# Optimization experiments

Measured on AMD Instinct MI355X. Metric: run time of the kernel, lower is better.

## Reference

```python
import jax, jax.numpy as jnp
import numpy as np

BETA = 0.25  # commitment_beta


def setup_inputs() -> dict:
    key = jax.random.key(0)
    k1, k2 = jax.random.split(key)
    x = jax.random.normal(k1, (16, 256, 32, 32), dtype=jnp.float32)
    # codebook weight: (n_embed + 1, embed_dim); last row is the padding idx (zeros)
    weight = jax.random.normal(k2, (8193, 256), dtype=jnp.float32) * 0.05
    weight = weight.at[-1].set(0.0)
    return {"x": x, "weight": weight}


def reference(x, weight):
    # Eval-mode forward of VectorQuantize2 (accept_image_fmap=True, no EMA update).
    B, C, H, W = x.shape
    xf = jnp.transpose(x, (0, 2, 3, 1)).reshape(B, H * W, C)  # b (h w) c
    emb = weight[:-1]  # [N, C], drop padding row
    # squared euclidean distance; argmin identical to torch.cdist argmin
    d2 = (
        jnp.sum(xf * xf, axis=-1, keepdims=True)
        - 2.0 * jnp.einsum("bnc,kc->bnk", xf, emb)
        + jnp.sum(emb * emb, axis=-1)
    )  # [B, HW, N]
    code = jnp.argmin(d2, axis=-1)  # [B, HW]
    x_q = emb[code]  # [B, HW, C]
    loss = BETA * jnp.mean((jax.lax.stop_gradient(x_q) - xf) ** 2) + jnp.mean(
        (x_q - jax.lax.stop_gradient(xf)) ** 2
    )
    # straight-through estimator
    xq_st = xf + jax.lax.stop_gradient(x_q - xf)
    xq_out = jnp.transpose(xq_st.reshape(B, H, W, C), (0, 3, 1, 2))  # b c h w
    code_out = code.reshape(B, H, W)
    return xq_out, loss, code_out
```

## Files before the change

### kernel.cpp

```cpp
#include <hip/hip_runtime.h>
#include <hip/hip_bf16.h>


#define N_ROWS   16384
#define KCODES   8192
#define DIM      256
#define LOSS_OFF 4194304
#define CODE_OFF 4194305
#define MARGIN_ACC 0.006f

typedef _Float16 half8  __attribute__((ext_vector_type(8)));
typedef _Float16 half4v __attribute__((ext_vector_type(4)));
typedef float    float4v __attribute__((ext_vector_type(4)));
typedef unsigned long long u64;

__device__ __forceinline__ unsigned umax32(unsigned a, unsigned b) { return a > b ? a : b; }
__device__ __forceinline__ unsigned umin32(unsigned a, unsigned b) { return a < b ? a : b; }
__device__ __forceinline__ void gll16(const _Float16* g, _Float16* l) {
  __builtin_amdgcn_global_load_lds((const __attribute__((address_space(1))) void*)g,
                                   (__attribute__((address_space(3))) void*)l, 16, 0, 0);
}

__device__ __forceinline__ void stage16k(const _Float16* __restrict__ g, _Float16* l, int t, int w) {
  gll16(g + t * 8,        l + w * 512);
  gll16(g + 4096 + t * 8, l + 4096 + w * 512);
}


__global__ __launch_bounds__(256) void k_prep(const float* __restrict__ x, _Float16* __restrict__ xh,
                                              const float* __restrict__ wt, _Float16* __restrict__ eh,
                                              float* __restrict__ en2c, float* __restrict__ sxxp,
                                              double* __restrict__ dacc, unsigned* __restrict__ cnt) {
  __shared__ float lsx[128 * 65];
  __shared__ __align__(16) _Float16 ls[8192];
  __shared__ float es[32];
  int t = threadIdx.x;
  int lane = t & 63, wv = t >> 6;
  int bid = blockIdx.x;
  if (bid < 512) {
    if (bid == 0 && t == 0) { dacc[0] = 0.0; *cnt = 0u; }
    int blk = bid >> 2, cc = bid & 3;
    int row0 = blk * 128;
    int b    = row0 >> 10;
    int n0   = row0 & 1023;
    const float* xb = x + (size_t)b * 262144 + n0;
    int n_l = t & 127, cg = t >> 7;
    float sxx = 0.f;
    for (int j = 0; j < 32; ++j) {
      int c = cc * 64 + cg * 32 + j;
      float v = xb[(size_t)c * 1024 + n_l];
      sxx = fmaf(v, v, sxx);
      lsx[n_l * 65 + (c & 63)] = v;
    }
    __syncthreads();
#pragma unroll
    for (int i = 0; i < 4; ++i) {
      int unit = i * 256 + t;
      int rl = unit >> 3, p = unit & 7;
      const float* src = &lsx[rl * 65 + p * 8];
      half8 h;
#pragma unroll
      for (int k2 = 0; k2 < 8; ++k2) h[k2] = (_Float16)src[k2];
      int p7 = p ^ (rl & 7);
      *(half8*)&xh[(size_t)blk * 32768 + (size_t)cc * 8192 + (size_t)rl * 64 + p7 * 8] = h;
    }
#pragma unroll
    for (int d = 32; d; d >>= 1) sxx += __shfl_xor(sxx, d);
    __syncthreads();
    if (lane == 0) lsx[wv] = sxx;
    __syncthreads();
    if (t == 0) sxxp[bid] = lsx[0] + lsx[1] + lsx[2] + lsx[3];
  } else {
    int blk  = bid - 512;
    int k0 = blk * 32;
    const float* wb = wt + (size_t)k0 * 256;
    for (int i = 0; i < 8; ++i) {
      int lin = i * 1024 + t * 4;
      float4v v = *(const float4v*)&wb[lin];
      half4v h; float ss = 0.f;
#pragma unroll
      for (int j = 0; j < 4; ++j) { h[j] = (_Float16)v[j]; ss = fmaf(v[j], v[j], ss); }
      *(half4v*)&ls[lin] = h;
#pragma unroll
      for (int d = 32; d; d >>= 1) ss += __shfl_xor(ss, d);
      if (lane == 0) es[i * 4 + wv] = ss;
    }
    __syncthreads();
    size_t tb = (size_t)(k0 >> 7) * 32768;
    for (int i = 0; i < 4; ++i) {
      int u = i * 256 + t;
      int code_l = u >> 5;
      int cu = u & 31, chunk = cu >> 3, p = cu & 7;
      int kgl = k0 + code_l;
      int kg = p ^ (kgl & 7);
      half8 h = *(half8*)&ls[code_l * 256 + chunk * 64 + kg * 8];
      *(half8*)&eh[tb + (size_t)chunk * 8192 + (size_t)(kgl & 127) * 64 + p * 8] = h;
    }
    if (t < 32) en2c[k0 + t] = 32.0f - 0.5f * es[t];
  }
}

__global__ __launch_bounds__(512, 2) void k_gemm(const _Float16* __restrict__ xh, const _Float16* __restrict__ eh,
                                                 const float* __restrict__ en2c,
                                                 u64* __restrict__ top2) {
  __shared__ __align__(16) _Float16 As[2][16384];
  __shared__ __align__(16) _Float16 Bs[2][16384];
  int t    = threadIdx.x;
  int lane = t & 63, w = t >> 6;
  int wr = w >> 2, wc = w & 3;
  int ln15 = lane & 15, q = (lane >> 4) & 3;
  int q4 = q * 4;

  int orig = (int)blockIdx.y * 32 + (int)blockIdx.x;
  int swz  = (orig & 7) * 256 + (orig >> 3);
  int bx = swz & 31;
  int by = swz >> 5;

  const _Float16* Ag0 = eh + (size_t)(2 * bx)     * 32768;
  const _Float16* Ag1 = eh + (size_t)(2 * bx + 1) * 32768;
  const _Float16* Bg0 = xh + (size_t)(2 * by)     * 32768;
  const _Float16* Bg1 = xh + (size_t)(2 * by + 1) * 32768;

  float4v acc[8][4];
#pragma unroll
  for (int mi = 0; mi < 8; ++mi) {
    float4v cin = *(const float4v*)&en2c[bx * 256 + wr * 128 + mi * 16 + q4];
#pragma unroll
    for (int ni = 0; ni < 4; ++ni) acc[mi][ni] = cin;
  }

  stage16k(Ag0, &As[0][0],    t, w);
  stage16k(Ag1, &As[0][8192], t, w);
  stage16k(Bg0, &Bs[0][0],    t, w);
  stage16k(Bg1, &Bs[0][8192], t, w);
  asm volatile("s_waitcnt vmcnt(0)" ::: "memory");
  __builtin_amdgcn_s_barrier();

#pragma unroll
  for (int kt = 0; kt < 4; ++kt) {
    const int d = kt & 1;
    const _Float16* Ac = &As[d][0];
    const _Float16* Bc = &Bs[d][0];
    _Float16* An = &As[d ^ 1][0];
    _Float16* Bn = &Bs[d ^ 1][0];
    half8 bf[4];
#pragma unroll
    for (int p = 0; p < 4; ++p) {
      const int ks = p >> 1, mih = p & 1;
      half8 af[4];
#pragma unroll
      for (int m2 = 0; m2 < 4; ++m2) {
        int rl = (mih * 4 + m2) * 16 + ln15;
        af[m2] = *(const half8*)&Ac[wr * 8192 + rl * 64 + (((ks * 4 + q) ^ (rl & 7)) * 8)];
      }
      if (mih == 0) {
#pragma unroll
        for (int ni = 0; ni < 4; ++ni) {
          int rb = (wc & 1) * 64 + ni * 16 + ln15;
          bf[ni] = *(const half8*)&Bc[(wc >> 1) * 8192 + rb * 64 + (((ks * 4 + q) ^ (rb & 7)) * 8)];
        }
      }
      if (kt < 3) {
        if (p == 0) stage16k(Ag0 + (kt + 1) * 8192, An,        t, w);
        if (p == 1) stage16k(Ag1 + (kt + 1) * 8192, An + 8192, t, w);
        if (p == 2) stage16k(Bg0 + (kt + 1) * 8192, Bn,        t, w);
        if (p == 3) stage16k(Bg1 + (kt + 1) * 8192, Bn + 8192, t, w);
      }
      __builtin_amdgcn_s_barrier();
      asm volatile("s_waitcnt lgkmcnt(0)");
      __builtin_amdgcn_s_setprio(1);
#pragma unroll
      for (int m2 = 0; m2 < 4; ++m2)
#pragma unroll
        for (int ni = 0; ni < 4; ++ni)
          acc[mih * 4 + m2][ni] =
              __builtin_amdgcn_mfma_f32_16x16x32_f16(af[m2], bf[ni], acc[mih * 4 + m2][ni], 0, 0, 0);
      __builtin_amdgcn_s_setprio(0);
      __builtin_amdgcn_s_barrier();
    }
    if (kt < 3) {
      asm volatile("s_waitcnt vmcnt(0)" ::: "memory");
      __builtin_amdgcn_sched_barrier(0);
      __builtin_amdgcn_s_barrier();
    }
  }

#pragma unroll
  for (int ni = 0; ni < 4; ++ni) {
    unsigned hi[16], lo2[16];
#pragma unroll
    for (int mi = 0; mi < 8; ++mi)
#pragma unroll
      for (int rb = 0; rb < 4; rb += 2) {
        int j = mi * 2 + (rb >> 1);
        unsigned p0 = (__float_as_uint(acc[mi][ni][rb])     & 0xFFFFFF80u) | (unsigned)(mi * 16 + q4 + rb);
        unsigned p1 = (__float_as_uint(acc[mi][ni][rb + 1]) & 0xFFFFFF80u) | (unsigned)(mi * 16 + q4 + rb + 1);
        hi[j] = umax32(p0, p1); lo2[j] = umin32(p0, p1);
      }
#pragma unroll
    for (int st = 8; st; st >>= 1)
#pragma unroll
      for (int j = 0; j < 8; ++j) if (j < st) {
        unsigned nb = umax32(hi[j], hi[j + st]);
        unsigned ns = umax32(umin32(hi[j], hi[j + st]), umax32(lo2[j], lo2[j + st]));
        hi[j] = nb; lo2[j] = ns;
      }
    unsigned b = hi[0], s = lo2[0];
#pragma unroll
    for (int dd = 16; dd < 64; dd <<= 1) {
      unsigned ob = __shfl_xor(b, dd);
      unsigned os = __shfl_xor(s, dd);
      unsigned ns = umax32(umin32(b, ob), umax32(s, os));
      b = umax32(b, ob); s = ns;
    }
    if (q == 0) {
      int row = by * 256 + wc * 64 + ni * 16 + ln15;
      top2[(size_t)(bx * 2 + wr) * 16384 + row] = ((u64)b << 32) | s;
    }
  }
}

__global__ __launch_bounds__(1024) void k_out(const u64* __restrict__ top2,
                                              const float* __restrict__ x, const float* __restrict__ w,
                                              float* __restrict__ out, const float* __restrict__ sxxp,
                                              double* __restrict__ dacc, unsigned* __restrict__ cnt) {
  __shared__ float ect[256 * 65];
  __shared__ double dpart[16];
  __shared__ unsigned oldc;
  int t    = threadIdx.x;
  int lane = t & 63, wv = t >> 6;
  int blk  = blockIdx.x;
  int row0 = blk * 64;
  int b = row0 >> 10, n0 = row0 & 1023;

  double dsum = 0.0;
  for (int j = 0; j < 4; ++j) {
    int rl  = wv * 4 + j;
    int row = row0 + rl;
    u64 e = top2[(size_t)lane * 16384 + row];
    unsigned hi = (unsigned)(e >> 32), lo = (unsigned)e;
    unsigned mx = hi;
#pragma unroll
    for (int d = 1; d < 64; d <<= 1) mx = umax32(mx, __shfl_xor(mx, d));
    float fm = __uint_as_float(mx & 0xFFFFFF80u);
    float th = fm - MARGIN_ACC;
    bool c0 = __uint_as_float(hi & 0xFFFFFF80u) >= th;
    bool c1 = __uint_as_float(lo & 0xFFFFFF80u) >= th;
    u64 bal0 = __ballot(c0), bal1 = __ballot(c1);
    int kbest;
    double d2c;
    if (__popcll(bal0) + __popcll(bal1) <= 1) {
      int l0 = __ffsll((unsigned long long)__ballot(hi == mx)) - 1;
      kbest = l0 * 128 + (int)(__shfl(hi, l0) & 127u);
      d2c = 64.0 - 2.0 * (double)fm;
    } else {
      const float* xr = x + (size_t)b * 262144 + (row & 1023);
      float4v ex;
#pragma unroll
      for (int i = 0; i < 4; ++i) ex[i] = xr[(size_t)(lane * 4 + i) * 1024];
      double bs = 1e300; int bk = 0x7fffffff;
      for (int pass = 0; pass < 2; ++pass) {
        u64 bal = pass ? bal1 : bal0;
        unsigned src = pass ? lo : hi;
        while (bal) {
          int l = __ffsll((unsigned long long)bal) - 1;
          bal &= bal - 1;
          int kc = l * 128 + (int)(__shfl(src, l) & 127u);
          float4v wv4 = *(const float4v*)&w[(size_t)kc * DIM + lane * 4];
          double s = 0.0;
#pragma unroll
          for (int i = 0; i < 4; ++i) { double ev = (double)wv4[i]; s += ev * (ev - 2.0 * (double)ex[i]); }
#pragma unroll
          for (int d = 1; d < 64; d <<= 1) s += __shfl_xor(s, d);
          if (s < bs || (s == bs && kc < bk)) { bs = s; bk = kc; }
        }
      }
      kbest = bk;
      d2c = bs;
    }
    if (lane == 0) { out[CODE_OFF + row] = (float)kbest; dsum += d2c; }
    const float* wrow = w + (size_t)kbest * 256;
#pragma unroll
    for (int i = 0; i < 4; ++i) ect[(i * 64 + lane) * 65 + rl] = wrow[i * 64 + lane];
  }
  __syncthreads();

  const size_t base = (size_t)b * 262144 + n0 + lane;
  for (int j = 0; j < 16; ++j) {
    int c = wv * 16 + j;
    out[base + (size_t)c * 1024] = ect[c * 65 + lane];
  }
  if (lane == 0) dpart[wv] = dsum;
  __syncthreads();
  if (t == 0) {
    double s = 0.0;
#pragma unroll
    for (int i = 0; i < 16; ++i) s += dpart[i];
    atomicAdd(&dacc[0], s);
    __threadfence();
    oldc = atomicAdd(cnt, 1u);
  }
  __syncthreads();
  if (oldc == 255u && t < 64) {
    float ps = 0.f;
#pragma unroll
    for (int i = 0; i < 8; ++i) ps += sxxp[t * 8 + i];
#pragma unroll
    for (int d = 32; d; d >>= 1) ps += __shfl_xor(ps, d);
    if (t == 0) {
      __threadfence();
      double sd2 = *(volatile double*)&dacc[0];
      out[LOSS_OFF] = (float)(1.25 * ((double)ps + sd2) / 4194304.0);
    }
  }
}

extern "C" void kernel_launch(void* const* d_in, const int* in_sizes, int n_in,
                              void* d_out, int out_size, void* d_ws, size_t ws_size,
                              hipStream_t stream) {
  const float* x = (const float*)d_in[0];
  const float* w = (const float*)d_in[1];
  float* out = (float*)d_out;
  char* ws = (char*)d_ws;
  _Float16* xh   = (_Float16*)(ws);
  _Float16* eh   = (_Float16*)(ws + 8388608);
  float*    en2c = (float*)(ws + 12582912);
  u64*      top2 = (u64*)(ws + 12615680);
  float*    sxxp = (float*)(ws + 21004288);
  double*   dacc = (double*)(ws + 21006336);
  unsigned* cnt  = (unsigned*)(ws + 21006344);

  k_prep<<<768, 256, 0, stream>>>(x, xh, w, eh, en2c, sxxp, dacc, cnt);
  k_gemm<<<dim3(32, 64), 512, 0, stream>>>(xh, eh, en2c, top2);
  k_out<<<256, 1024, 0, stream>>>(top2, x, w, out, sxxp, dacc, cnt);
}
```

Baseline: 186.2 us.

## Make GEMM persistent over eight row tiles with cross-tile prefetch

The distance GEMM now launches 256 persistent blocks instead of 2048. Each block keeps one codebook column tile and loops over eight row tiles assigned by XCD index. The next tile's A and B panels are prefetched during the last k-step of the current tile, which hides per-block launch and prologue costs. Separately, the prep kernel loads x as float2 pairs to widen global loads. The persistent form reloads the A panel for every tile and may leave CUs underused if 256 blocks at 2 per CU do not balance well.

```diff
diff --git a/kernel.cpp b/kernel.cpp
--- a/kernel.cpp
+++ b/kernel.cpp
@@ -12,6 +12,7 @@
 typedef _Float16 half8  __attribute__((ext_vector_type(8)));
 typedef _Float16 half4v __attribute__((ext_vector_type(4)));
 typedef float    float4v __attribute__((ext_vector_type(4)));
+typedef float    float2v __attribute__((ext_vector_type(2)));
 typedef unsigned long long u64;
 
 __device__ __forceinline__ unsigned umax32(unsigned a, unsigned b) { return a > b ? a : b; }
@@ -44,13 +45,17 @@
     int b    = row0 >> 10;
     int n0   = row0 & 1023;
     const float* xb = x + (size_t)b * 262144 + n0;
-    int n_l = t & 127, cg = t >> 7;
+    int c_off = t >> 6;
+    int nn    = (t & 63) * 2;
     float sxx = 0.f;
-    for (int j = 0; j < 32; ++j) {
-      int c = cc * 64 + cg * 32 + j;
-      float v = xb[(size_t)c * 1024 + n_l];
-      sxx = fmaf(v, v, sxx);
-      lsx[n_l * 65 + (c & 63)] = v;
+    for (int j = 0; j < 16; ++j) {
+      int c = cc * 64 + j * 4 + c_off;
+      float2v v = *(const float2v*)&xb[(size_t)c * 1024 + nn];
+      int cp = c & 63;
+      sxx = fmaf(v[0], v[0], sxx);
+      sxx = fmaf(v[1], v[1], sxx);
+      lsx[nn * 65 + cp]       = v[0];
+      lsx[(nn + 1) * 65 + cp] = v[1];
     }
     __syncthreads();
 #pragma unroll
@@ -111,111 +116,136 @@
   int ln15 = lane & 15, q = (lane >> 4) & 3;
   int q4 = q * 4;
 
-  int orig = (int)blockIdx.y * 32 + (int)blockIdx.x;
-  int swz  = (orig & 7) * 256 + (orig >> 3);
-  int bx = swz & 31;
-  int by = swz >> 5;
-
-  const _Float16* Ag0 = eh + (size_t)(2 * bx)     * 32768;
-  const _Float16* Ag1 = eh + (size_t)(2 * bx + 1) * 32768;
-  const _Float16* Bg0 = xh + (size_t)(2 * by)     * 32768;
-  const _Float16* Bg1 = xh + (size_t)(2 * by + 1) * 32768;
+  int p   = (int)blockIdx.x;
+  int xcd = p & 7;
+  int bx  = p >> 3;
+
+  const _Float16* Ag0 = eh + (size_t)(2 * bx) * 32768;
+  const _Float16* Ag1 = Ag0 + 32768;
+  const float*    cb  = &en2c[bx * 256 + wr * 128 + q4];
 
   float4v acc[8][4];
 #pragma unroll
   for (int mi = 0; mi < 8; ++mi) {
-    float4v cin = *(const float4v*)&en2c[bx * 256 + wr * 128 + mi * 16 + q4];
+    float4v cin = *(const float4v*)&cb[mi * 16];
 #pragma unroll
     for (int ni = 0; ni < 4; ++ni) acc[mi][ni] = cin;
   }
 
+  const _Float16* Bg0f = xh + (size_t)(2 * (xcd * 8)) * 32768;
   stage16k(Ag0, &As[0][0],    t, w);
   stage16k(Ag1, &As[0][8192], t, w);
-  stage16k(Bg0, &Bs[0][0],    t, w);
-  stage16k(Bg1, &Bs[0][8192], t, w);
+  stage16k(Bg0f,         &Bs[0][0],    t, w);
+  stage16k(Bg0f + 32768, &Bs[0][8192], t, w);
   asm volatile("s_waitcnt vmcnt(0)" ::: "memory");
   __builtin_amdgcn_s_barrier();
 
-#pragma unroll
-  for (int kt = 0; kt < 4; ++kt) {
-    const int d = kt & 1;
-    const _Float16* Ac = &As[d][0];
-    const _Float16* Bc = &Bs[d][0];
-    _Float16* An = &As[d ^ 1][0];
-    _Float16* Bn = &Bs[d ^ 1][0];
-    half8 bf[4];
-#pragma unroll
-    for (int p = 0; p < 4; ++p) {
-      const int ks = p >> 1, mih = p & 1;
-      half8 af[4];
-#pragma unroll
-      for (int m2 = 0; m2 < 4; ++m2) {
-        int rl = (mih * 4 + m2) * 16 + ln15;
-        af[m2] = *(const half8*)&Ac[wr * 8192 + rl * 64 + (((ks * 4 + q) ^ (rl & 7)) * 8)];
-      }
-      if (mih == 0) {
-#pragma unroll
-        for (int ni = 0; ni < 4; ++ni) {
-          int rb = (wc & 1) * 64 + ni * 16 + ln15;
-          bf[ni] = *(const half8*)&Bc[(wc >> 1) * 8192 + rb * 64 + (((ks * 4 + q) ^ (rb & 7)) * 8)];
-        }
+#pragma unroll 1
+  for (int s = 0; s < 8; ++s) {
+    int by = xcd * 8 + s;
+    const _Float16* Bg0 = xh + (size_t)(2 * by) * 32768;
+    const _Float16* Bg1 = Bg0 + 32768;
+    const _Float16* Bn0 = Bg0 + 65536;
+    const _Float16* Bn1 = Bn0 + 32768;
+
+#pragma unroll
+    for (int kt = 0; kt < 4; ++kt) {
+      const int d = kt & 1;
+      const _Float16* Ac = &As[d][0];
+      const _Float16* Bc = &Bs[d][0];
+      _Float16* An = &As[d ^ 1][0];
+      _Float16* Bn = &Bs[d ^ 1][0];
+      half8 bf[4];
+#pragma unroll
+      for (int ph = 0; ph < 4; ++ph) {
+        const int ks = ph >> 1, mih = ph & 1;
+        half8 af[4];
+#pragma unroll
+        for (int m2 = 0; m2 < 4; ++m2) {
+          int rl = (mih * 4 + m2) * 16 + ln15;
+          af[m2] = *(const half8*)&Ac[wr * 8192 + rl * 64 + (((ks * 4 + q) ^ (rl & 7)) * 8)];
+        }
+        if (mih == 0) {
+#pragma unroll
+          for (int ni = 0; ni < 4; ++ni) {
+            int rb = (wc & 1) * 64 + ni * 16 + ln15;
+            bf[ni] = *(const half8*)&Bc[(wc >> 1) * 8192 + rb * 64 + (((ks * 4 + q) ^ (rb & 7)) * 8)];
+          }
+        }
+        if (kt < 3) {
+          if (ph == 0) stage16k(Ag0 + (kt + 1) * 8192, An,        t, w);
+          if (ph == 1) stage16k(Ag1 + (kt + 1) * 8192, An + 8192, t, w);
+          if (ph == 2) stage16k(Bg0 + (kt + 1) * 8192, Bn,        t, w);
+          if (ph == 3) stage16k(Bg1 + (kt + 1) * 8192, Bn + 8192, t, w);
+        } else if (s < 7) {
+          if (ph == 0) stage16k(Ag0, An,        t, w);
+          if (ph == 1) stage16k(Ag1, An + 8192, t, w);
+          if (ph == 2) stage16k(Bn0, Bn,        t, w);
+          if (ph == 3) stage16k(Bn1, Bn + 8192, t, w);
+        }
+        __builtin_amdgcn_s_barrier();
+        asm volatile("s_waitcnt lgkmcnt(0)");
+        __builtin_amdgcn_s_setprio(1);
+#pragma unroll
+        for (int m2 = 0; m2 < 4; ++m2)
+#pragma unroll
+          for (int ni = 0; ni < 4; ++ni)
+            acc[mih * 4 + m2][ni] =
+                __builtin_amdgcn_mfma_f32_16x16x32_f16(af[m2], bf[ni], acc[mih * 4 + m2][ni], 0, 0, 0);
+        __builtin_amdgcn_s_setprio(0);
+        __builtin_amdgcn_s_barrier();
       }
       if (kt < 3) {
-        if (p == 0) stage16k(Ag0 + (kt + 1) * 8192, An,        t, w);
-        if (p == 1) stage16k(Ag1 + (kt + 1) * 8192, An + 8192, t, w);
-        if (p == 2) stage16k(Bg0 + (kt + 1) * 8192, Bn,        t, w);
-        if (p == 3) stage16k(Bg1 + (kt + 1) * 8192, Bn + 8192, t, w);
-      }
-      __builtin_amdgcn_s_barrier();
-      asm volatile("s_waitcnt lgkmcnt(0)");
-      __builtin_amdgcn_s_setprio(1);
-#pragma unroll
-      for (int m2 = 0; m2 < 4; ++m2)
-#pragma unroll
-        for (int ni = 0; ni < 4; ++ni)
-          acc[mih * 4 + m2][ni] =
-              __builtin_amdgcn_mfma_f32_16x16x32_f16(af[m2], bf[ni], acc[mih * 4 + m2][ni], 0, 0, 0);
-      __builtin_amdgcn_s_setprio(0);
-      __builtin_amdgcn_s_barrier();
-    }
-    if (kt < 3) {
+        asm volatile("s_waitcnt vmcnt(0)" ::: "memory");
+        __builtin_amdgcn_sched_barrier(0);
+        __builtin_amdgcn_s_barrier();
+      }
+    }
+
+#pragma unroll
+    for (int ni = 0; ni < 4; ++ni) {
+      unsigned hi[16], lo2[16];
+#pragma unroll
+      for (int mi = 0; mi < 8; ++mi)
+#pragma unroll
+        for (int rb = 0; rb < 4; rb += 2) {
+          int j = mi * 2 + (rb >> 1);
+          unsigned p0 = (__float_as_uint(acc[mi][ni][rb])     & 0xFFFFFF80u) | (unsigned)(mi * 16 + q4 + rb);
+          unsigned p1 = (__float_as_uint(acc[mi][ni][rb + 1]) & 0xFFFFFF80u) | (unsigned)(mi * 16 + q4 + rb + 1);
+          hi[j] = umax32(p0, p1); lo2[j] = umin32(p0, p1);
+        }
+#pragma unroll
+      for (int st = 8; st; st >>= 1)
+#pragma unroll
+        for (int j = 0; j < 8; ++j) if (j < st) {
+          unsigned nb = umax32(hi[j], hi[j + st]);
+          unsigned ns = umax32(umin32(hi[j], hi[j + st]), umax32(lo2[j], lo2[j + st]));
+          hi[j] = nb; lo2[j] = ns;
+        }
+      unsigned b = hi[0], sv = lo2[0];
+#pragma unroll
+      for (int dd = 16; dd < 64; dd <<= 1) {
+        unsigned ob = __shfl_xor(b, dd);
+        unsigned os = __shfl_xor(sv, dd);
+        unsigned ns = umax32(umin32(b, ob), umax32(sv, os));
+        b = umax32(b, ob); sv = ns;
+      }
+      if (q == 0) {
+        int row = by * 256 + wc * 64 + ni * 16 + ln15;
+        top2[(size_t)(bx * 2 + wr) * 16384 + row] = ((u64)b << 32) | sv;
+      }
+    }
+
+    if (s < 7) {
+#pragma unroll
+      for (int mi = 0; mi < 8; ++mi) {
+        float4v cin = *(const float4v*)&cb[mi * 16];
+#pragma unroll
+        for (int ni = 0; ni < 4; ++ni) acc[mi][ni] = cin;
+      }
       asm volatile("s_waitcnt vmcnt(0)" ::: "memory");
       __builtin_amdgcn_sched_barrier(0);
       __builtin_amdgcn_s_barrier();
-    }
-  }
-
-#pragma unroll
-  for (int ni = 0; ni < 4; ++ni) {
-    unsigned hi[16], lo2[16];
-#pragma unroll
-    for (int mi = 0; mi < 8; ++mi)
-#pragma unroll
-      for (int rb = 0; rb < 4; rb += 2) {
-        int j = mi * 2 + (rb >> 1);
-        unsigned p0 = (__float_as_uint(acc[mi][ni][rb])     & 0xFFFFFF80u) | (unsigned)(mi * 16 + q4 + rb);
-        unsigned p1 = (__float_as_uint(acc[mi][ni][rb + 1]) & 0xFFFFFF80u) | (unsigned)(mi * 16 + q4 + rb + 1);
-        hi[j] = umax32(p0, p1); lo2[j] = umin32(p0, p1);
-      }
-#pragma unroll
-    for (int st = 8; st; st >>= 1)
-#pragma unroll
-      for (int j = 0; j < 8; ++j) if (j < st) {
-        unsigned nb = umax32(hi[j], hi[j + st]);
-        unsigned ns = umax32(umin32(hi[j], hi[j + st]), umax32(lo2[j], lo2[j + st]));
-        hi[j] = nb; lo2[j] = ns;
-      }
-    unsigned b = hi[0], s = lo2[0];
-#pragma unroll
-    for (int dd = 16; dd < 64; dd <<= 1) {
-      unsigned ob = __shfl_xor(b, dd);
-      unsigned os = __shfl_xor(s, dd);
-      unsigned ns = umax32(umin32(b, ob), umax32(s, os));
-      b = umax32(b, ob); s = ns;
-    }
-    if (q == 0) {
-      int row = by * 256 + wc * 64 + ni * 16 + ln15;
-      top2[(size_t)(bx * 2 + wr) * 16384 + row] = ((u64)b << 32) | s;
     }
   }
 }
@@ -331,6 +361,6 @@
   unsigned* cnt  = (unsigned*)(ws + 21006344);
 
   k_prep<<<768, 256, 0, stream>>>(x, xh, w, eh, en2c, sxxp, dacc, cnt);
-  k_gemm<<<dim3(32, 64), 512, 0, stream>>>(xh, eh, en2c, top2);
+  k_gemm<<<256, 512, 0, stream>>>(xh, eh, en2c, top2);
   k_out<<<256, 1024, 0, stream>>>(top2, x, w, out, sxxp, dacc, cnt);
 }
```

New measurement: 228.0 us. +22.4%, slower.
